# Kernel tuning notes

Measured on AMD Instinct MI355X. Metric: run time of the kernel, lower is better.

Reference implementation:

```python
import jax, jax.numpy as jnp
import numpy as np

D_K = 64

def setup_inputs() -> dict:
    key = jax.random.key(0)
    kq, kk, kv, km = jax.random.split(key, 4)
    B, H, S, D = 8, 12, 1024, D_K
    Q = jax.random.normal(kq, (B, H, S, D), dtype=jnp.float32)
    K = jax.random.normal(kk, (B, H, S, D), dtype=jnp.float32)
    V = jax.random.normal(kv, (B, H, S, D), dtype=jnp.float32)
    # boolean mask: True = masked out (as used by masked_fill_)
    attn_mask = jax.random.randint(km, (B, H, S, S), 0, 2) == 1
    return {"Q": Q, "K": K, "V": V, "attn_mask": attn_mask}

def reference(Q, K, V, attn_mask):
    # scores: [B, H, S, S]
    scale = 1.0 / np.sqrt(D_K).astype(np.float32)
    scores = jnp.einsum('bhqd,bhkd->bhqk', Q, K) * scale
    scores = jnp.where(attn_mask, jnp.float32(-1e9), scores)
    attn = jax.nn.softmax(scores, axis=-1)
    context = jnp.einsum('bhqk,bhkd->bhqd', attn, V)
    return (context, attn)
```

## Files before the change

kernel.cpp:

```cpp
#include <hip/hip_runtime.h>

#define S_LEN  1024
#define D_KK   64
#define N_HEAD 96

#define TK 256
#define BQ 16

__global__ __launch_bounds__(256, 2) void attn_softmax_kernel(
    const float* __restrict__ Qg, const float* __restrict__ Kg,
    const int* __restrict__ maskg, float* __restrict__ attng)
{
    __shared__ float kt[D_KK][TK + 1];
    __shared__ float qs[BQ][68];

    const int t    = threadIdx.x;
    const int lane = t & 63;
    const int wave = t >> 6;
    const int head = blockIdx.y;
    const int q0   = blockIdx.x * BQ;
    const int rbase = wave << 2;

    {
        const int r  = t >> 4;
        const int d0 = (t & 15) << 2;
        const float4 qv = *(const float4*)(Qg + ((size_t)head * S_LEN + q0 + r) * D_KK + d0);
        qs[r][d0 + 0] = qv.x; qs[r][d0 + 1] = qv.y;
        qs[r][d0 + 2] = qv.z; qs[r][d0 + 3] = qv.w;
    }

    float s[4][16];

    for (int kt_i = 0; kt_i < S_LEN / TK; ++kt_i) {
        __syncthreads();
        {
            const int d0 = (t & 15) << 2;
            const int kb = t >> 4;
            #pragma unroll
            for (int c = 0; c < TK / 16; ++c) {
                const int kl = c * 16 + kb;
                const float4 kv = *(const float4*)(Kg + ((size_t)head * S_LEN + kt_i * TK + kl) * D_KK + d0);
                kt[d0 + 0][kl] = kv.x;
                kt[d0 + 1][kl] = kv.y;
                kt[d0 + 2][kl] = kv.z;
                kt[d0 + 3][kl] = kv.w;
            }
        }
        __syncthreads();

        float acc[4][4] = {{0.f,0.f,0.f,0.f},{0.f,0.f,0.f,0.f},
                           {0.f,0.f,0.f,0.f},{0.f,0.f,0.f,0.f}};
        for (int d0 = 0; d0 < D_KK; d0 += 4) {
            float4 qv[4];
            #pragma unroll
            for (int r = 0; r < 4; ++r)
                qv[r] = *(const float4*)(&qs[rbase + r][d0]);
            #pragma unroll
            for (int dd = 0; dd < 4; ++dd) {
                float kv[4];
                #pragma unroll
                for (int j = 0; j < 4; ++j)
                    kv[j] = kt[d0 + dd][lane + 64 * j];
                #pragma unroll
                for (int r = 0; r < 4; ++r) {
                    const float qd = (&qv[r].x)[dd];
                    #pragma unroll
                    for (int j = 0; j < 4; ++j)
                        acc[r][j] = fmaf(qd, kv[j], acc[r][j]);
                }
            }
        }
        #pragma unroll
        for (int r = 0; r < 4; ++r)
            #pragma unroll
            for (int j = 0; j < 4; ++j)
                s[r][kt_i * 4 + j] = acc[r][j] * 0.125f;
    }

    #pragma unroll
    for (int r = 0; r < 4; ++r) {
        const int q = q0 + rbase + r;
        const int*  mrow = maskg + ((size_t)head * S_LEN + q) * S_LEN;
        float*      arow = attng + ((size_t)head * S_LEN + q) * S_LEN;
        float m = -3.0e38f;
        #pragma unroll
        for (int j = 0; j < 16; ++j) {
            if (mrow[lane + 64 * j]) s[r][j] = -1.0e9f;
            m = fmaxf(m, s[r][j]);
        }
        #pragma unroll
        for (int off = 32; off >= 1; off >>= 1)
            m = fmaxf(m, __shfl_xor(m, off, 64));
        float l = 0.0f;
        #pragma unroll
        for (int j = 0; j < 16; ++j) {
            s[r][j] = __expf(s[r][j] - m);
            l += s[r][j];
        }
        #pragma unroll
        for (int off = 32; off >= 1; off >>= 1)
            l += __shfl_xor(l, off, 64);
        const float inv = 1.0f / l;
        #pragma unroll
        for (int j = 0; j < 16; ++j)
            arow[lane + 64 * j] = s[r][j] * inv;
    }
}

#define TKB 128

__global__ __launch_bounds__(256, 2) void attn_pv_kernel(
    const float* __restrict__ attng, const float* __restrict__ Vg,
    float* __restrict__ ctxg)
{
    __shared__ float at[64][132];
    __shared__ float vt[TKB][68];

    const int t    = threadIdx.x;
    const int tx   = t & 15;
    const int ty   = t >> 4;
    const int head = blockIdx.y;
    const int q0   = blockIdx.x * 64;

    float acc[4][4] = {{0.f,0.f,0.f,0.f},{0.f,0.f,0.f,0.f},
                       {0.f,0.f,0.f,0.f},{0.f,0.f,0.f,0.f}};

    for (int k0 = 0; k0 < S_LEN; k0 += TKB) {
        __syncthreads();
        #pragma unroll
        for (int p = 0; p < 8; ++p) {
            const int i  = t + 256 * p;
            const int q  = i >> 5;
            const int kk = (i & 31) << 2;
            const float4 a = *(const float4*)(attng + ((size_t)head * S_LEN + q0 + q) * S_LEN + k0 + kk);
            *(float4*)(&at[q][kk]) = a;
        }
        #pragma unroll
        for (int p = 0; p < 8; ++p) {
            const int i  = t + 256 * p;
            const int k  = i >> 4;
            const int d0 = (i & 15) << 2;
            const float4 v = *(const float4*)(Vg + ((size_t)head * S_LEN + k0 + k) * D_KK + d0);
            *(float4*)(&vt[k][d0]) = v;
        }
        __syncthreads();

        for (int k = 0; k < TKB; ++k) {
            const float4 v = *(const float4*)(&vt[k][tx << 2]);
            #pragma unroll
            for (int qq = 0; qq < 4; ++qq) {
                const float a = at[(ty << 2) + qq][k];
                acc[qq][0] = fmaf(a, v.x, acc[qq][0]);
                acc[qq][1] = fmaf(a, v.y, acc[qq][1]);
                acc[qq][2] = fmaf(a, v.z, acc[qq][2]);
                acc[qq][3] = fmaf(a, v.w, acc[qq][3]);
            }
        }
    }

    #pragma unroll
    for (int qq = 0; qq < 4; ++qq) {
        float4 o;
        o.x = acc[qq][0]; o.y = acc[qq][1]; o.z = acc[qq][2]; o.w = acc[qq][3];
        *(float4*)(ctxg + ((size_t)head * S_LEN + q0 + (ty << 2) + qq) * D_KK + (tx << 2)) = o;
    }
}

extern "C" void kernel_launch(void* const* d_in, const int* in_sizes, int n_in,
                              void* d_out, int out_size, void* d_ws, size_t ws_size,
                              hipStream_t stream) {
    const float* Q    = (const float*)d_in[0];
    const float* K    = (const float*)d_in[1];
    const float* V    = (const float*)d_in[2];
    const int*   mask = (const int*)d_in[3];

    float* ctx  = (float*)d_out;
    float* attn = ctx + (size_t)N_HEAD * S_LEN * D_KK;

    dim3 gridA(S_LEN / BQ, N_HEAD);
    attn_softmax_kernel<<<gridA, 256, 0, stream>>>(Q, K, mask, attn);

    dim3 gridB(S_LEN / 64, N_HEAD);
    attn_pv_kernel<<<gridB, 256, 0, stream>>>(attn, V, ctx);
}
```

Measured before the change: 1.042 ms.

## Fuse softmax and PV into one kernel keeping probabilities in registers

Merges the QK/softmax kernel and the PV kernel into a single kernel. The normalized probabilities stay in registers and are staged through shared memory for the PV product, so the attention matrix is no longer re-read from global memory. The QK tile shrinks to 128 keys, accumulation goes directly into the score registers, and mask loads and attn stores use nontemporal hints. Occupancy is requested at 4 blocks, but each 16-query block must reload all of V, which adds V traffic, and the PV stage may be less efficient than the earlier 64-query tiling.

Result: slower. 1.351 ms (+29.7%).

```diff
diff --git a/kernel.cpp b/kernel.cpp
--- a/kernel.cpp
+++ b/kernel.cpp
@@ -3,35 +3,44 @@
 #define S_LEN  1024
 #define D_KK   64
 #define N_HEAD 96
+#define BQ     16
+#define TK     128
+#define NT_QK  (S_LEN / TK)
+#define NCHUNK (S_LEN / 64)
 
-#define TK 256
-#define BQ 16
+__global__ __launch_bounds__(256, 4) void attn_fused_kernel(
+    const float* __restrict__ Qg, const float* __restrict__ Kg,
+    const float* __restrict__ Vg, const int* __restrict__ maskg,
+    float* __restrict__ attng, float* __restrict__ ctxg)
+{
+    __shared__ float smA[64 * 129];
+    __shared__ float smB[16 * 68];
 
-__global__ __launch_bounds__(256, 2) void attn_softmax_kernel(
-    const float* __restrict__ Qg, const float* __restrict__ Kg,
-    const int* __restrict__ maskg, float* __restrict__ attng)
-{
-    __shared__ float kt[D_KK][TK + 1];
-    __shared__ float qs[BQ][68];
-
-    const int t    = threadIdx.x;
-    const int lane = t & 63;
-    const int wave = t >> 6;
-    const int head = blockIdx.y;
-    const int q0   = blockIdx.x * BQ;
+    const int t     = threadIdx.x;
+    const int lane  = t & 63;
+    const int wave  = t >> 6;
+    const int head  = blockIdx.y;
+    const int q0    = blockIdx.x * BQ;
     const int rbase = wave << 2;
 
     {
         const int r  = t >> 4;
         const int d0 = (t & 15) << 2;
         const float4 qv = *(const float4*)(Qg + ((size_t)head * S_LEN + q0 + r) * D_KK + d0);
-        qs[r][d0 + 0] = qv.x; qs[r][d0 + 1] = qv.y;
-        qs[r][d0 + 2] = qv.z; qs[r][d0 + 3] = qv.w;
+        smB[r * 68 + d0 + 0] = qv.x;
+        smB[r * 68 + d0 + 1] = qv.y;
+        smB[r * 68 + d0 + 2] = qv.z;
+        smB[r * 68 + d0 + 3] = qv.w;
     }
 
     float s[4][16];
+    #pragma unroll
+    for (int r = 0; r < 4; ++r)
+        #pragma unroll
+        for (int j = 0; j < 16; ++j) s[r][j] = 0.f;
 
-    for (int kt_i = 0; kt_i < S_LEN / TK; ++kt_i) {
+    #pragma unroll
+    for (int kt_i = 0; kt_i < NT_QK; ++kt_i) {
         __syncthreads();
         {
             const int d0 = (t & 15) << 2;
@@ -40,41 +49,32 @@
             for (int c = 0; c < TK / 16; ++c) {
                 const int kl = c * 16 + kb;
                 const float4 kv = *(const float4*)(Kg + ((size_t)head * S_LEN + kt_i * TK + kl) * D_KK + d0);
-                kt[d0 + 0][kl] = kv.x;
-                kt[d0 + 1][kl] = kv.y;
-                kt[d0 + 2][kl] = kv.z;
-                kt[d0 + 3][kl] = kv.w;
+                smA[(d0 + 0) * 129 + kl] = kv.x;
+                smA[(d0 + 1) * 129 + kl] = kv.y;
+                smA[(d0 + 2) * 129 + kl] = kv.z;
+                smA[(d0 + 3) * 129 + kl] = kv.w;
             }
         }
         __syncthreads();
 
-        float acc[4][4] = {{0.f,0.f,0.f,0.f},{0.f,0.f,0.f,0.f},
-                           {0.f,0.f,0.f,0.f},{0.f,0.f,0.f,0.f}};
+        #pragma unroll
         for (int d0 = 0; d0 < D_KK; d0 += 4) {
             float4 qv[4];
             #pragma unroll
             for (int r = 0; r < 4; ++r)
-                qv[r] = *(const float4*)(&qs[rbase + r][d0]);
+                qv[r] = *(const float4*)(&smB[(rbase + r) * 68 + d0]);
             #pragma unroll
             for (int dd = 0; dd < 4; ++dd) {
-                float kv[4];
-                #pragma unroll
-                for (int j = 0; j < 4; ++j)
-                    kv[j] = kt[d0 + dd][lane + 64 * j];
+                const float k0v = smA[(d0 + dd) * 129 + lane];
+                const float k1v = smA[(d0 + dd) * 129 + lane + 64];
                 #pragma unroll
                 for (int r = 0; r < 4; ++r) {
                     const float qd = (&qv[r].x)[dd];
-                    #pragma unroll
-                    for (int j = 0; j < 4; ++j)
-                        acc[r][j] = fmaf(qd, kv[j], acc[r][j]);
+                    s[r][2 * kt_i + 0] = fmaf(qd, k0v, s[r][2 * kt_i + 0]);
+                    s[r][2 * kt_i + 1] = fmaf(qd, k1v, s[r][2 * kt_i + 1]);
                 }
             }
         }
-        #pragma unroll
-        for (int r = 0; r < 4; ++r)
-            #pragma unroll
-            for (int j = 0; j < 4; ++j)
-                s[r][kt_i * 4 + j] = acc[r][j] * 0.125f;
     }
 
     #pragma unroll
@@ -85,8 +85,11 @@
         float m = -3.0e38f;
         #pragma unroll
         for (int j = 0; j < 16; ++j) {
-            if (mrow[lane + 64 * j]) s[r][j] = -1.0e9f;
-            m = fmaxf(m, s[r][j]);
+            const int mk = __builtin_nontemporal_load(&mrow[lane + 64 * j]);
+            float v = s[r][j] * 0.125f;
+            if (mk) v = -1.0e9f;
+            s[r][j] = v;
+            m = fmaxf(m, v);
         }
         #pragma unroll
         for (int off = 32; off >= 1; off >>= 1)
@@ -102,68 +105,49 @@
             l += __shfl_xor(l, off, 64);
         const float inv = 1.0f / l;
         #pragma unroll
-        for (int j = 0; j < 16; ++j)
-            arow[lane + 64 * j] = s[r][j] * inv;
+        for (int j = 0; j < 16; ++j) {
+            s[r][j] *= inv;
+            __builtin_nontemporal_store(s[r][j], &arow[lane + 64 * j]);
+        }
     }
-}
 
-#define TKB 128
+    float acc0 = 0.f, acc1 = 0.f, acc2 = 0.f, acc3 = 0.f;
+    const int qr = lane >> 4;
+    const int tx = lane & 15;
 
-__global__ __launch_bounds__(256, 2) void attn_pv_kernel(
-    const float* __restrict__ attng, const float* __restrict__ Vg,
-    float* __restrict__ ctxg)
-{
-    __shared__ float at[64][132];
-    __shared__ float vt[TKB][68];
-
-    const int t    = threadIdx.x;
-    const int tx   = t & 15;
-    const int ty   = t >> 4;
-    const int head = blockIdx.y;
-    const int q0   = blockIdx.x * 64;
-
-    float acc[4][4] = {{0.f,0.f,0.f,0.f},{0.f,0.f,0.f,0.f},
-                       {0.f,0.f,0.f,0.f},{0.f,0.f,0.f,0.f}};
-
-    for (int k0 = 0; k0 < S_LEN; k0 += TKB) {
+    #pragma unroll
+    for (int c2 = 0; c2 < NCHUNK; ++c2) {
         __syncthreads();
         #pragma unroll
-        for (int p = 0; p < 8; ++p) {
-            const int i  = t + 256 * p;
-            const int q  = i >> 5;
-            const int kk = (i & 31) << 2;
-            const float4 a = *(const float4*)(attng + ((size_t)head * S_LEN + q0 + q) * S_LEN + k0 + kk);
-            *(float4*)(&at[q][kk]) = a;
+        for (int p_ = 0; p_ < 4; ++p_) {
+            const int i  = t + 256 * p_;
+            const int k  = i >> 4;
+            const int d0 = (i & 15) << 2;
+            const float4 v = *(const float4*)(Vg + ((size_t)head * S_LEN + c2 * 64 + k) * D_KK + d0);
+            *(float4*)(&smA[k * 68 + d0]) = v;
         }
         #pragma unroll
-        for (int p = 0; p < 8; ++p) {
-            const int i  = t + 256 * p;
-            const int k  = i >> 4;
-            const int d0 = (i & 15) << 2;
-            const float4 v = *(const float4*)(Vg + ((size_t)head * S_LEN + k0 + k) * D_KK + d0);
-            *(float4*)(&vt[k][d0]) = v;
-        }
+        for (int r = 0; r < 4; ++r)
+            smB[(rbase + r) * 68 + lane] = s[r][c2];
         __syncthreads();
 
-        for (int k = 0; k < TKB; ++k) {
-            const float4 v = *(const float4*)(&vt[k][tx << 2]);
+        #pragma unroll
+        for (int kk = 0; kk < 16; ++kk) {
+            const float4 a4 = *(const float4*)(&smB[(rbase + qr) * 68 + 4 * kk]);
             #pragma unroll
-            for (int qq = 0; qq < 4; ++qq) {
-                const float a = at[(ty << 2) + qq][k];
-                acc[qq][0] = fmaf(a, v.x, acc[qq][0]);
-                acc[qq][1] = fmaf(a, v.y, acc[qq][1]);
-                acc[qq][2] = fmaf(a, v.z, acc[qq][2]);
-                acc[qq][3] = fmaf(a, v.w, acc[qq][3]);
+            for (int e = 0; e < 4; ++e) {
+                const float  a = (&a4.x)[e];
+                const float4 v = *(const float4*)(&smA[(4 * kk + e) * 68 + (tx << 2)]);
+                acc0 = fmaf(a, v.x, acc0);
+                acc1 = fmaf(a, v.y, acc1);
+                acc2 = fmaf(a, v.z, acc2);
+                acc3 = fmaf(a, v.w, acc3);
             }
         }
     }
 
-    #pragma unroll
-    for (int qq = 0; qq < 4; ++qq) {
-        float4 o;
-        o.x = acc[qq][0]; o.y = acc[qq][1]; o.z = acc[qq][2]; o.w = acc[qq][3];
-        *(float4*)(ctxg + ((size_t)head * S_LEN + q0 + (ty << 2) + qq) * D_KK + (tx << 2)) = o;
-    }
+    float4 o; o.x = acc0; o.y = acc1; o.z = acc2; o.w = acc3;
+    *(float4*)(ctxg + ((size_t)head * S_LEN + q0 + rbase + qr) * D_KK + (tx << 2)) = o;
 }
 
 extern "C" void kernel_launch(void* const* d_in, const int* in_sizes, int n_in,
@@ -177,9 +161,6 @@
     float* ctx  = (float*)d_out;
     float* attn = ctx + (size_t)N_HEAD * S_LEN * D_KK;
 
-    dim3 gridA(S_LEN / BQ, N_HEAD);
-    attn_softmax_kernel<<<gridA, 256, 0, stream>>>(Q, K, mask, attn);
-
-    dim3 gridB(S_LEN / 64, N_HEAD);
-    attn_pv_kernel<<<gridB, 256, 0, stream>>>(attn, V, ctx);
+    dim3 grid(S_LEN / BQ, N_HEAD);
+    attn_fused_kernel<<<grid, 256, 0, stream>>>(Q, K, V, mask, attn, ctx);
 }
```
